# Kernel tuning notes

Measured on AMD Instinct MI355X. Metric: run time of the kernel, lower is better.

The kernel has to match this reference:

```python
import jax, jax.numpy as jnp
import numpy as np

B = 64          # graphs in batch
NPG = 9         # nodes per graph (max_atoms = NUM_ATOMS = 9)
N = B * NPG     # total nodes = 576
H = 128         # node_dim == hid_dim
SPEC_LEN = 1801
SPEC_COMP = 100
BOND = 3
ASL = BOND * 9 * 9  # action_space_length = 243


def _linear_init(key, fan_in, fan_out):
    # torch.nn.Linear default init: U(-1/sqrt(fan_in), 1/sqrt(fan_in)); stored as [in, out]
    kw, kb = jax.random.split(key)
    bound = 1.0 / np.sqrt(fan_in)
    W = jax.random.uniform(kw, (fan_in, fan_out), jnp.float32, -bound, bound)
    b = jax.random.uniform(kb, (fan_out,), jnp.float32, -bound, bound)
    return W, b


def setup_inputs() -> dict:
    key = jax.random.key(0)
    ks = jax.random.split(key, 10)
    node_features = jax.random.normal(ks[0], (N, H), jnp.float32)
    specs = jax.random.normal(ks[1], (B, 1, SPEC_LEN), jnp.float32)
    # len_vec[b, i] = 1 iff node i belongs to graph b (contiguous 9-node blocks)
    gid = np.repeat(np.arange(B), NPG)
    len_vec = jnp.asarray((gid[None, :] == np.arange(B)[:, None]).astype(np.float32))
    mask = jnp.zeros((B, ASL), jnp.float32)  # additive action mask (0 = allowed)
    indexmask = jax.random.randint(ks[2], (B, ASL), 0, ASL, dtype=jnp.int32)
    W1, b1 = _linear_init(ks[3], SPEC_LEN, SPEC_LEN // 2)
    W2, b2 = _linear_init(ks[4], SPEC_LEN // 2, SPEC_COMP)
    Wv1, bv1 = _linear_init(ks[5], H + SPEC_COMP, H // 2)
    Wv2, bv2 = _linear_init(ks[6], H // 2, 1)
    Wa2, ba2 = _linear_init(ks[7], 2 * H + SPEC_COMP, H)
    Wf, bf = _linear_init(ks[8], H, BOND)
    return {"node_features": node_features, "specs": specs, "len_vec": len_vec,
            "mask": mask, "indexmask": indexmask,
            "W1": W1, "b1": b1, "W2": W2, "b2": b2,
            "Wv1": Wv1, "bv1": bv1, "Wv2": Wv2, "bv2": bv2,
            "Wa2": Wa2, "ba2": ba2, "Wf": Wf, "bf": bf}


def reference(node_features, specs, len_vec, mask, indexmask,
              W1, b1, W2, b2, Wv1, bv1, Wv2, bv2, Wa2, ba2, Wf, bf):
    relu = jax.nn.relu
    n_total, hdim = node_features.shape
    bsz = specs.shape[0]
    npg = n_total // bsz

    # --- spectrum compression: [B,1801] -> [B,100] ---
    s = relu(specs[:, 0, :] @ W1 + b1)
    s = relu(s @ W2 + b2)

    # --- value head: SumPooling readout + spec -> scalar per graph ---
    readout = node_features.reshape(bsz, npg, hdim).sum(axis=1)
    v = relu(jnp.concatenate([readout, s], axis=-1) @ Wv1 + bv1) @ Wv2 + bv2  # [B,1]

    # --- pairwise action features ---
    # original: apf[i,j] = relu(cat(nf[i], nf[j], canvas[i,j])) then Linear(action_2).
    # relu is elementwise and Linear splits over the concat, so factorize:
    #   apf @ Wa2 = relu(nf)[i] @ Wa2[:H]  +  relu(nf)[j] @ Wa2[H:2H]  +  relu(canvas)[i,j] @ Wa2[2H:]
    # canvas is the block-diagonal scatter of s (s >= 0 so relu(canvas) = canvas).
    gid = jnp.arange(n_total) // npg
    same = gid[:, None] == gid[None, :]          # block-diagonal [N,N]
    nf_r = relu(node_features)
    Ai = nf_r @ Wa2[:hdim]                        # [N,H] per-row (Y2) term
    Bj = nf_r @ Wa2[hdim:2 * hdim]                # [N,H] per-col (X2) term
    D = s @ Wa2[2 * hdim:]                        # [B,H] spec-canvas term
    h = relu(Ai[:, None, :] + Bj[None, :, :]
             + jnp.where(same[:, :, None], D[gid][:, None, :], 0.0) + ba2)  # [N,N,H]

    len_matrix = (len_vec.T @ len_vec)[:, :, None]  # block-diagonal pair mask [N,N,1]
    saf = (h @ Wf + bf) * len_matrix                # [N,N,BOND]

    # --- per-graph action assembly (replaces nonzero()+pad+index_select loop) ---
    # with npg nodes per graph the nonzeros of saf are exactly the diagonal
    # npg x npg blocks, flattened (i, j, bond)-major, npg*npg*BOND == ASL.
    rows = jnp.arange(bsz)[:, None] * npg + jnp.arange(npg)[None, :]   # [B,npg]
    fp = saf[rows[:, :, None], rows[:, None, :], :].reshape(bsz, npg * npg * saf.shape[-1])
    gathered = jnp.take_along_axis(fp, indexmask.astype(jnp.int32), axis=1)
    return jax.nn.softmax(gathered + mask, axis=1), v
```

## Files before the change

### kernel.cpp

```cpp
#include <hip/hip_runtime.h>
#include <math.h>

#define BATCH 64
#define NPG 9
#define N_NODES 576
#define HD 128
#define SPEC_LEN 1801
#define S1DIM 900
#define SCOMP 100
#define ASL 243
#define NT 15
#define KC 17
#define KCH 106
#define KPAD 112

__global__ __launch_bounds__(256) void k1(const float* __restrict__ specs,
                                          const float* __restrict__ W1,
                                          const float* __restrict__ nf,
                                          const float* __restrict__ Wa2,
                                          float* __restrict__ P,
                                          float* __restrict__ AB) {
    int bb = blockIdx.x, tid = threadIdx.x;
    if (bb < NT * KC) {
        __shared__ __align__(16) float sA[KPAD * 68];
        __shared__ __align__(16) float sB[KPAD * 64];
        int nt = bb % NT, kc = bb / NT;
        int n0 = nt * 64, kb = kc * KCH;
        int klen = min(KCH, SPEC_LEN - kb);

#pragma unroll
        for (int p = 0; p < 28; ++p) {
            int e = p * 256 + tid;
            int m = e / KPAD;
            int k = e - m * KPAD;
            float v = (k < klen) ? specs[(size_t)m * SPEC_LEN + kb + k] : 0.0f;
            sA[k * 68 + m] = v;
        }
#pragma unroll
        for (int p = 0; p < 7; ++p) {
            int e = p * 256 + tid;
            int kl = e >> 4, nq = (e & 15) * 4;
            float4 v = make_float4(0.f, 0.f, 0.f, 0.f);
            if (kl < klen && (n0 + nq) < S1DIM)
                v = *(const float4*)&W1[(size_t)(kb + kl) * S1DIM + n0 + nq];
            *(float4*)&sB[kl * 64 + nq] = v;
        }
        __syncthreads();

        int tn = (tid & 15) * 4;
        int tm = (tid >> 4) * 4;
        float acc[4][4] = {};
#pragma unroll 4
        for (int k = 0; k < KPAD; ++k) {
            const float4 a = *(const float4*)&sA[k * 68 + tm];
            const float4 b = *(const float4*)&sB[k * 64 + tn];
            acc[0][0] = fmaf(a.x, b.x, acc[0][0]);
            acc[0][1] = fmaf(a.x, b.y, acc[0][1]);
            acc[0][2] = fmaf(a.x, b.z, acc[0][2]);
            acc[0][3] = fmaf(a.x, b.w, acc[0][3]);
            acc[1][0] = fmaf(a.y, b.x, acc[1][0]);
            acc[1][1] = fmaf(a.y, b.y, acc[1][1]);
            acc[1][2] = fmaf(a.y, b.z, acc[1][2]);
            acc[1][3] = fmaf(a.y, b.w, acc[1][3]);
            acc[2][0] = fmaf(a.z, b.x, acc[2][0]);
            acc[2][1] = fmaf(a.z, b.y, acc[2][1]);
            acc[2][2] = fmaf(a.z, b.z, acc[2][2]);
            acc[2][3] = fmaf(a.z, b.w, acc[2][3]);
            acc[3][0] = fmaf(a.w, b.x, acc[3][0]);
            acc[3][1] = fmaf(a.w, b.y, acc[3][1]);
            acc[3][2] = fmaf(a.w, b.z, acc[3][2]);
            acc[3][3] = fmaf(a.w, b.w, acc[3][3]);
        }

        if (n0 + tn < S1DIM) {
#pragma unroll
            for (int i = 0; i < 4; ++i) {
                float4 o = make_float4(acc[i][0], acc[i][1], acc[i][2], acc[i][3]);
                *(float4*)&P[((size_t)(kc * 64 + tm + i)) * S1DIM + n0 + tn] = o;
            }
        }
    } else {
        __shared__ float snf[4 * HD];
        int ib = (bb - NT * KC) * 4;
        snf[tid]       = fmaxf(nf[(size_t)ib * HD + tid], 0.0f);
        snf[256 + tid] = fmaxf(nf[(size_t)ib * HD + 256 + tid], 0.0f);
        __syncthreads();
        int c = tid;
        const float* __restrict__ wp = (c < HD) ? (Wa2 + c) : (Wa2 + HD * HD + (c - HD));
        float a0 = 0.f, a1 = 0.f, a2 = 0.f, a3 = 0.f;
#pragma unroll 16
        for (int k = 0; k < HD; ++k) {
            float w = wp[(size_t)k * HD];
            a0 = fmaf(snf[k], w, a0);
            a1 = fmaf(snf[HD + k], w, a1);
            a2 = fmaf(snf[2 * HD + k], w, a2);
            a3 = fmaf(snf[3 * HD + k], w, a3);
        }
        AB[(size_t)(ib + 0) * 256 + c] = a0;
        AB[(size_t)(ib + 1) * 256 + c] = a1;
        AB[(size_t)(ib + 2) * 256 + c] = a2;
        AB[(size_t)(ib + 3) * 256 + c] = a3;
    }
}

__global__ __launch_bounds__(256) void k2(const float* __restrict__ P,
                                          const float* __restrict__ b1,
                                          const float* __restrict__ W2,
                                          const float* __restrict__ b2,
                                          const float* __restrict__ Wa2,
                                          const float* __restrict__ nf,
                                          const float* __restrict__ Wv1,
                                          const float* __restrict__ bv1,
                                          const float* __restrict__ Wv2,
                                          const float* __restrict__ bv2,
                                          const float* __restrict__ ba2,
                                          const float* __restrict__ Wf,
                                          const float* __restrict__ bfb,
                                          const int* __restrict__ indexmask,
                                          const float* __restrict__ mask,
                                          const float* __restrict__ AB,
                                          float* __restrict__ out,
                                          float* __restrict__ vout) {
    int m = blockIdx.x, tid = threadIdx.x;
    __shared__ __align__(16) float s1row[S1DIM];
    __shared__ __align__(16) float sAi[NPG * 132];
    __shared__ __align__(16) float sBj[NPG * 132];
    __shared__ __align__(16) float sWfT[3 * 132];
    __shared__ __align__(16) float srow[SCOMP];
    __shared__ __align__(16) float ro[HD];
    __shared__ __align__(16) float sC[HD];
    __shared__ float part[200];
    __shared__ float fp[ASL];
    __shared__ float red[8];

    for (int n = tid; n < S1DIM; n += 256) {
        float a = b1[n];
#pragma unroll
        for (int kc = 0; kc < KC; ++kc)
            a += P[((size_t)kc * 64 + m) * S1DIM + n];
        s1row[n] = fmaxf(a, 0.0f);
    }
    for (int e = tid; e < NPG * 256; e += 256) {
        int i = e >> 8, c = e & 255;
        float v = AB[(size_t)(m * NPG + i) * 256 + c];
        if (c < HD) sAi[i * 132 + c] = v;
        else        sBj[i * 132 + (c - HD)] = v;
    }
    for (int e = tid; e < 3 * HD; e += 256)
        sWfT[(e % 3) * 132 + (e / 3)] = Wf[e];
    if (tid >= 128) {
        int h = tid - 128;
        float a = 0.0f;
#pragma unroll
        for (int i = 0; i < NPG; ++i) a += nf[(size_t)(m * NPG + i) * HD + h];
        ro[h] = a;
    }
    __syncthreads();

    if (tid < 200) {
        int c = tid % 100;
        int kb = (tid / 100) * 450;
        float a = 0.0f;
#pragma unroll 10
        for (int kl = 0; kl < 450; ++kl)
            a = fmaf(s1row[kb + kl], W2[(size_t)(kb + kl) * SCOMP + c], a);
        part[tid] = a;
    }
    __syncthreads();
    if (tid < SCOMP) srow[tid] = fmaxf(part[tid] + part[tid + 100] + b2[tid], 0.0f);
    __syncthreads();

    if (tid < HD) {
        float a = 0.0f;
#pragma unroll 10
        for (int k = 0; k < SCOMP; ++k)
            a = fmaf(srow[k], Wa2[(size_t)(2 * HD + k) * HD + tid], a);
        sC[tid] = a + ba2[tid];
    } else if (tid < 192) {
        int t = tid - 128;
        float a = bv1[t];
#pragma unroll 8
        for (int k = 0; k < HD; ++k) a = fmaf(ro[k], Wv1[(size_t)k * 64 + t], a);
#pragma unroll 10
        for (int k = 0; k < SCOMP; ++k) a = fmaf(srow[k], Wv1[(size_t)(HD + k) * 64 + t], a);
        a = fmaxf(a, 0.0f);
        float p = a * Wv2[t];
#pragma unroll
        for (int off = 32; off; off >>= 1) p += __shfl_down(p, off, 64);
        if (tid == 128) vout[m] = p + bv2[0];
    }
    __syncthreads();

    if (tid < ASL) {
        int i = tid / 27;
        int j = (tid / 3) % 9;
        int bo = tid % 3;
        float a = bfb[bo];
        const float* pa = sAi + i * 132;
        const float* pb = sBj + j * 132;
        const float* pw = sWfT + bo * 132;
#pragma unroll 8
        for (int h = 0; h < HD; h += 4) {
            const float4 A = *(const float4*)&pa[h];
            const float4 Bv = *(const float4*)&pb[h];
            const float4 C = *(const float4*)&sC[h];
            const float4 W = *(const float4*)&pw[h];
            a = fmaf(fmaxf(A.x + Bv.x + C.x, 0.f), W.x, a);
            a = fmaf(fmaxf(A.y + Bv.y + C.y, 0.f), W.y, a);
            a = fmaf(fmaxf(A.z + Bv.z + C.z, 0.f), W.z, a);
            a = fmaf(fmaxf(A.w + Bv.w + C.w, 0.f), W.w, a);
        }
        fp[tid] = a;
    }
    __syncthreads();

    float g = -INFINITY;
    if (tid < ASL) g = fp[indexmask[(size_t)m * ASL + tid]] + mask[(size_t)m * ASL + tid];
    float mx = g;
#pragma unroll
    for (int off = 32; off; off >>= 1) mx = fmaxf(mx, __shfl_down(mx, off, 64));
    if ((tid & 63) == 0) red[tid >> 6] = mx;
    __syncthreads();
    mx = fmaxf(fmaxf(red[0], red[1]), fmaxf(red[2], red[3]));
    float e = (tid < ASL) ? __expf(g - mx) : 0.0f;
    float sm = e;
#pragma unroll
    for (int off = 32; off; off >>= 1) sm += __shfl_down(sm, off, 64);
    if ((tid & 63) == 0) red[4 + (tid >> 6)] = sm;
    __syncthreads();
    sm = red[4] + red[5] + red[6] + red[7];
    if (tid < ASL) out[(size_t)m * ASL + tid] = e / sm;
}

extern "C" void kernel_launch(void* const* d_in, const int* in_sizes, int n_in,
                              void* d_out, int out_size, void* d_ws, size_t ws_size,
                              hipStream_t stream) {
    (void)in_sizes; (void)n_in; (void)out_size; (void)ws_size;
    const float* nf    = (const float*)d_in[0];
    const float* specs = (const float*)d_in[1];
    const float* mask  = (const float*)d_in[3];
    const int*   idxm  = (const int*)d_in[4];
    const float* W1  = (const float*)d_in[5];
    const float* b1  = (const float*)d_in[6];
    const float* W2  = (const float*)d_in[7];
    const float* b2  = (const float*)d_in[8];
    const float* Wv1 = (const float*)d_in[9];
    const float* bv1 = (const float*)d_in[10];
    const float* Wv2 = (const float*)d_in[11];
    const float* bv2 = (const float*)d_in[12];
    const float* Wa2 = (const float*)d_in[13];
    const float* ba2 = (const float*)d_in[14];
    const float* Wf  = (const float*)d_in[15];
    const float* bfv = (const float*)d_in[16];
    float* out = (float*)d_out;
    float* ws  = (float*)d_ws;

    float* P  = ws;
    float* AB = P + (size_t)KC * 64 * S1DIM;

    k1<<<dim3(NT * KC + N_NODES / 4), dim3(256), 0, stream>>>(specs, W1, nf, Wa2, P, AB);
    k2<<<dim3(BATCH), dim3(256), 0, stream>>>(P, b1, W2, b2, Wa2, nf,
                                              Wv1, bv1, Wv2, bv2, ba2, Wf, bfv,
                                              idxm, mask, AB, out, out + BATCH * ASL);
}
```

Measured before the change: 138.4 us.

## Split spectrum second layer into separate kernel parallelized over K chunks

The split-K reduction of the first spectrum layer and the 900x100 second-layer matmul move out of the 64-block tail kernel into a new kernel launched on a 64x9 grid. Each block reduces its 100-wide K slice and writes a partial result, and the tail kernel sums the 9 partials. The tail kernel also splits its D and value-head matvecs across all 256 threads with partial sums, where before only a subset of threads did the work. The aim is to raise parallelism in what was a serial, latency-bound stage, at the cost of one extra launch and a global round trip for the partials.

```diff
diff --git a/kernel.cpp b/kernel.cpp
--- a/kernel.cpp
+++ b/kernel.cpp
@@ -103,9 +103,32 @@
     }
 }
 
-__global__ __launch_bounds__(256) void k2(const float* __restrict__ P,
+__global__ __launch_bounds__(128) void k2(const float* __restrict__ P,
                                           const float* __restrict__ b1,
                                           const float* __restrict__ W2,
+                                          float* __restrict__ Pc) {
+    __shared__ float sld[100];
+    int m = blockIdx.x, kc9 = blockIdx.y, tid = threadIdx.x;
+    int kb = kc9 * 100;
+    if (tid < 100) {
+        int k = kb + tid;
+        float a = b1[k];
+#pragma unroll
+        for (int kc = 0; kc < KC; ++kc)
+            a += P[((size_t)kc * 64 + m) * S1DIM + k];
+        sld[tid] = fmaxf(a, 0.0f);
+    }
+    __syncthreads();
+    if (tid < SCOMP) {
+        float a = 0.0f;
+#pragma unroll 10
+        for (int kl = 0; kl < 100; ++kl)
+            a = fmaf(sld[kl], W2[(size_t)(kb + kl) * SCOMP + tid], a);
+        Pc[((size_t)kc9 * 64 + m) * SCOMP + tid] = a;
+    }
+}
+
+__global__ __launch_bounds__(256) void k3(const float* __restrict__ Pc,
                                           const float* __restrict__ b2,
                                           const float* __restrict__ Wa2,
                                           const float* __restrict__ nf,
@@ -122,24 +145,17 @@
                                           float* __restrict__ out,
                                           float* __restrict__ vout) {
     int m = blockIdx.x, tid = threadIdx.x;
-    __shared__ __align__(16) float s1row[S1DIM];
     __shared__ __align__(16) float sAi[NPG * 132];
     __shared__ __align__(16) float sBj[NPG * 132];
     __shared__ __align__(16) float sWfT[3 * 132];
-    __shared__ __align__(16) float srow[SCOMP];
-    __shared__ __align__(16) float ro[HD];
+    __shared__ __align__(16) float rv[232];
     __shared__ __align__(16) float sC[HD];
-    __shared__ float part[200];
+    __shared__ float pD[256];
+    __shared__ float pV[256];
     __shared__ float fp[ASL];
     __shared__ float red[8];
 
-    for (int n = tid; n < S1DIM; n += 256) {
-        float a = b1[n];
-#pragma unroll
-        for (int kc = 0; kc < KC; ++kc)
-            a += P[((size_t)kc * 64 + m) * S1DIM + n];
-        s1row[n] = fmaxf(a, 0.0f);
-    }
+#pragma unroll
     for (int e = tid; e < NPG * 256; e += 256) {
         int i = e >> 8, c = e & 255;
         float v = AB[(size_t)(m * NPG + i) * 256 + c];
@@ -148,42 +164,46 @@
     }
     for (int e = tid; e < 3 * HD; e += 256)
         sWfT[(e % 3) * 132 + (e / 3)] = Wf[e];
+    if (tid < SCOMP) {
+        float a = b2[tid];
+#pragma unroll
+        for (int q = 0; q < 9; ++q)
+            a += Pc[((size_t)q * 64 + m) * SCOMP + tid];
+        rv[128 + tid] = fmaxf(a, 0.0f);
+    }
     if (tid >= 128) {
         int h = tid - 128;
         float a = 0.0f;
 #pragma unroll
         for (int i = 0; i < NPG; ++i) a += nf[(size_t)(m * NPG + i) * HD + h];
-        ro[h] = a;
-    }
-    __syncthreads();
-
-    if (tid < 200) {
-        int c = tid % 100;
-        int kb = (tid / 100) * 450;
-        float a = 0.0f;
+        rv[h] = a;
+    }
+    __syncthreads();
+
+    {
+        int t = tid & 127, half = tid >> 7;
+        float aD = 0.0f;
 #pragma unroll 10
-        for (int kl = 0; kl < 450; ++kl)
-            a = fmaf(s1row[kb + kl], W2[(size_t)(kb + kl) * SCOMP + c], a);
-        part[tid] = a;
-    }
-    __syncthreads();
-    if (tid < SCOMP) srow[tid] = fmaxf(part[tid] + part[tid + 100] + b2[tid], 0.0f);
-    __syncthreads();
-
+        for (int kl = 0; kl < 50; ++kl) {
+            int k = half * 50 + kl;
+            aD = fmaf(rv[128 + k], Wa2[(size_t)(2 * HD + k) * HD + t], aD);
+        }
+        pD[tid] = aD;
+        int tv = tid & 63, q = tid >> 6;
+        float aV = 0.0f;
+#pragma unroll 8
+        for (int kl = 0; kl < 57; ++kl) {
+            int k = q * 57 + kl;
+            aV = fmaf(rv[k], Wv1[(size_t)k * 64 + tv], aV);
+        }
+        pV[tid] = aV;
+    }
+    __syncthreads();
     if (tid < HD) {
-        float a = 0.0f;
-#pragma unroll 10
-        for (int k = 0; k < SCOMP; ++k)
-            a = fmaf(srow[k], Wa2[(size_t)(2 * HD + k) * HD + tid], a);
-        sC[tid] = a + ba2[tid];
+        sC[tid] = pD[tid] + pD[tid + 128] + ba2[tid];
     } else if (tid < 192) {
         int t = tid - 128;
-        float a = bv1[t];
-#pragma unroll 8
-        for (int k = 0; k < HD; ++k) a = fmaf(ro[k], Wv1[(size_t)k * 64 + t], a);
-#pragma unroll 10
-        for (int k = 0; k < SCOMP; ++k) a = fmaf(srow[k], Wv1[(size_t)(HD + k) * 64 + t], a);
-        a = fmaxf(a, 0.0f);
+        float a = fmaxf(pV[t] + pV[64 + t] + pV[128 + t] + pV[192 + t] + bv1[t], 0.0f);
         float p = a * Wv2[t];
 #pragma unroll
         for (int off = 32; off; off >>= 1) p += __shfl_down(p, off, 64);
@@ -257,9 +277,11 @@
 
     float* P  = ws;
     float* AB = P + (size_t)KC * 64 * S1DIM;
+    float* Pc = AB + (size_t)N_NODES * 256;
 
     k1<<<dim3(NT * KC + N_NODES / 4), dim3(256), 0, stream>>>(specs, W1, nf, Wa2, P, AB);
-    k2<<<dim3(BATCH), dim3(256), 0, stream>>>(P, b1, W2, b2, Wa2, nf,
+    k2<<<dim3(BATCH, 9), dim3(128), 0, stream>>>(P, b1, W2, Pc);
+    k3<<<dim3(BATCH), dim3(256), 0, stream>>>(Pc, b2, Wa2, nf,
                                               Wv1, bv1, Wv2, bv2, ba2, Wf, bfv,
                                               idxm, mask, AB, out, out + BATCH * ASL);
 }
```

New measurement: 127.8 us. -7.7%, faster.
